# Kernel tuning notes

Measured on AMD Instinct MI355X. Metric: run time of the kernel, lower is better.

The kernel has to match this reference:

```python
import jax, jax.numpy as jnp
import numpy as np

BS, LS, HS, P, M, V, D = 16, 128, 768, 8, 1024, 20000, 512
T = BS * LS
N_POS_TOTAL = 12   # pos ids >= P are non-target (copied through)
N_PRIVACY = 4      # pos ids < N_PRIVACY count as privacy terms
TEMP = 1.0


def setup_inputs() -> dict:
    key = jax.random.key(0)
    ks = jax.random.split(key, 8)
    return {
        "inp_word": jax.random.randint(ks[0], (BS, LS), 0, V),
        "inp_pos": jax.random.randint(ks[1], (BS, LS), 0, N_POS_TOTAL),
        "inp_mask": jnp.ones((BS, LS), dtype=bool),
        "ctx": jax.random.normal(ks[2], (BS, LS, HS), dtype=jnp.float32),
        "dec_W": jax.random.normal(ks[3], (P, HS, M), dtype=jnp.float32) * 0.05,
        "dec_b": jnp.zeros((P, M), dtype=jnp.float32),
        "psr_weight": jax.random.normal(ks[4], (V, D), dtype=jnp.float32) * 0.1,
        "atk_weight": jax.random.normal(ks[5], (V, D), dtype=jnp.float32) * 0.1,
        "words": jax.random.randint(ks[6], (P, M), 0, V),
        "u_gumbel": jax.random.uniform(ks[7], (T, M), dtype=jnp.float32),
    }


def reference(inp_word, inp_pos, inp_mask, ctx, dec_W, dec_b,
              psr_weight, atk_weight, words, u_gumbel):
    bs, ls = inp_word.shape
    t_tok = bs * ls
    wordf = inp_word.reshape(t_tok)          # [T]
    posf = inp_pos.reshape(t_tok)            # [T]
    ctxf = ctx.reshape(t_tok, -1)            # [T, hs]

    # per-expert decode: Linear + LogSoftmax over each expert's sub-vocab
    logits = jnp.einsum('th,phm->ptm', ctxf, dec_W) + dec_b[:, None, :]  # [P,T,M]
    pspt = jax.nn.log_softmax(logits, axis=-1)                            # [P,T,M]

    # entropy: for each POS, mean of -pspt*exp(pspt) over its masked tokens
    neg_ent = -(pspt * jnp.exp(pspt)).sum(-1)                 # [P,T]
    pm = posf[None, :] == jnp.arange(P)[:, None]              # [P,T] token->expert mask
    n_p = pm.sum(1)                                           # [P]
    ent_p = (neg_ent * pm).sum(1) / (jnp.maximum(n_p, 1) * M)
    entropy = jnp.where(n_p > 0, ent_p, 0.0).sum()

    # gumbel-softmax sample (soft), one noise draw per token
    u = jnp.clip(u_gumbel, 1e-6, 1.0 - 1e-6)
    g = -jnp.log(-jnp.log(u))                                 # [T,M]
    spt = jax.nn.softmax((pspt + g[None]) / TEMP, axis=-1)    # [P,T,M]

    # hard word choice + soft embedding mix
    idx = jnp.argmax(spt, axis=-1)                            # [P,T]
    spt_word = jnp.take_along_axis(words, idx, axis=1)        # [P,T]
    psr_lut = psr_weight[words]                               # [P,M,D]
    atk_lut = atk_weight[words]                               # [P,M,D]
    psr_e = jnp.einsum('ptm,pmd->ptd', spt, psr_lut)          # [P,T,D]
    atk_e = jnp.einsum('ptm,pmd->ptd', spt, atk_lut)          # [P,T,D]

    # combine: each token takes its own POS expert's output (scatter)
    tmask = posf < P                                          # [T] obfuscated tokens
    sel = jnp.where(tmask, posf, 0)                           # [T] expert id
    ar = jnp.arange(t_tok)
    obf_wordf = jnp.where(tmask, spt_word[sel, ar], wordf)
    obf_psr = jnp.where(tmask[:, None], psr_e[sel, ar], psr_weight[wordf])
    obf_atk = jnp.where(tmask[:, None], atk_e[sel, ar], atk_weight[wordf])

    obf_word = obf_wordf.reshape(bs, ls)
    obf_psr_emb = obf_psr.reshape(bs, ls, -1)
    obf_atk_emb = obf_atk.reshape(bs, ls, -1)
    cpy_mask = (obf_word == inp_word) & inp_mask
    obf_mask = tmask.reshape(bs, ls)
    pri_mask = (inp_pos < N_PRIVACY) & obf_mask
    ent_loss = -entropy
    return obf_word, obf_psr_emb, obf_atk_emb, ent_loss, cpy_mask, obf_mask, pri_mask
```

## Files before the change

### kernel.cpp

```cpp
#include <hip/hip_runtime.h>
#include <cstdint>

#define BSZ   16
#define LSEQ  128
#define HS    768
#define NEXP  8
#define MM    1024
#define DD    512
#define TT    (BSZ*LSEQ)
#define NPRIV 4

#define OFF_WORD 0
#define OFF_PSR  2048
#define OFF_ATK  (2048 + 2048*512)
#define OFF_ENT  (OFF_ATK + 2048*512)
#define OFF_CPY  (OFF_ENT + 1)
#define OFF_OBF  (OFF_CPY + 2048)
#define OFF_PRI  (OFF_OBF + 2048)

#define WS_SPT      0
#define WS_TOKLIST  (TT*MM*4)
#define WS_CNT      (WS_TOKLIST + NEXP*TT*4)
#define WS_ENTSUM   (WS_CNT + NEXP*4)

__global__ void k_bucket(const int* __restrict__ pos,
                         int* __restrict__ toklist, int* __restrict__ cnt)
{
  int t = blockIdx.x * blockDim.x + threadIdx.x;
  if (t >= TT) return;
  int p = pos[t];
  if (p < NEXP) {
    int r = atomicAdd(&cnt[p], 1);
    toklist[p * TT + r] = t;
  }
}

#define TM1 32
#define TN1 128
#define TK1 64

__global__ __launch_bounds__(256) void k_decode(
    const float* __restrict__ ctx, const float* __restrict__ dec_W,
    const float* __restrict__ dec_b, const int* __restrict__ toklist,
    const int* __restrict__ cnt, float* __restrict__ logits)
{
  const int p = blockIdx.z;
  const int ncnt = cnt[p];
  const int row0 = blockIdx.y * TM1;
  if (row0 >= ncnt) return;
  const int n0 = blockIdx.x * TN1;
  const int tid = threadIdx.x;

  __shared__ float sA[TM1][TK1 + 1];
  __shared__ float sB[TK1][TN1];

  const int tx = tid & 31, ty = tid >> 5;
  const int tx4 = tx * 4, ty4 = ty * 4;

  const int ar = tid >> 3;
  const int ac0 = (tid & 7) * 8;
  int tA = -1;
  if (row0 + ar < ncnt) tA = toklist[p * TT + row0 + ar];

  const int br = tid >> 5;
  const int bc4 = (tid & 31) * 4;

  int tO[4];
  #pragma unroll
  for (int i = 0; i < 4; ++i) {
    int rr = row0 + ty4 + i;
    tO[i] = (rr < ncnt) ? toklist[p * TT + rr] : -1;
  }

  float acc[4][4] = {};

  for (int k0 = 0; k0 < HS; k0 += TK1) {
    if (tA >= 0) {
      const float* src = ctx + (size_t)tA * HS + k0 + ac0;
      #pragma unroll
      for (int j = 0; j < 8; ++j) sA[ar][ac0 + j] = src[j];
    } else {
      #pragma unroll
      for (int j = 0; j < 8; ++j) sA[ar][ac0 + j] = 0.f;
    }
    const float* wbase = dec_W + ((size_t)p * HS + k0) * MM + n0;
    #pragma unroll
    for (int j = 0; j < 8; ++j) {
      *(float4*)&sB[br + j * 8][bc4] =
          *(const float4*)(wbase + (size_t)(br + j * 8) * MM + bc4);
    }
    __syncthreads();
    #pragma unroll 8
    for (int kk = 0; kk < TK1; ++kk) {
      const float a0 = sA[ty4 + 0][kk];
      const float a1 = sA[ty4 + 1][kk];
      const float a2 = sA[ty4 + 2][kk];
      const float a3 = sA[ty4 + 3][kk];
      const float4 b = *(const float4*)&sB[kk][tx4];
      acc[0][0] = fmaf(a0, b.x, acc[0][0]); acc[0][1] = fmaf(a0, b.y, acc[0][1]);
      acc[0][2] = fmaf(a0, b.z, acc[0][2]); acc[0][3] = fmaf(a0, b.w, acc[0][3]);
      acc[1][0] = fmaf(a1, b.x, acc[1][0]); acc[1][1] = fmaf(a1, b.y, acc[1][1]);
      acc[1][2] = fmaf(a1, b.z, acc[1][2]); acc[1][3] = fmaf(a1, b.w, acc[1][3]);
      acc[2][0] = fmaf(a2, b.x, acc[2][0]); acc[2][1] = fmaf(a2, b.y, acc[2][1]);
      acc[2][2] = fmaf(a2, b.z, acc[2][2]); acc[2][3] = fmaf(a2, b.w, acc[2][3]);
      acc[3][0] = fmaf(a3, b.x, acc[3][0]); acc[3][1] = fmaf(a3, b.y, acc[3][1]);
      acc[3][2] = fmaf(a3, b.z, acc[3][2]); acc[3][3] = fmaf(a3, b.w, acc[3][3]);
    }
    __syncthreads();
  }

  const float4 bv = *(const float4*)(dec_b + (size_t)p * MM + n0 + tx4);
  #pragma unroll
  for (int i = 0; i < 4; ++i) {
    if (tO[i] >= 0) {
      float4 o;
      o.x = acc[i][0] + bv.x; o.y = acc[i][1] + bv.y;
      o.z = acc[i][2] + bv.z; o.w = acc[i][3] + bv.w;
      *(float4*)(logits + (size_t)tO[i] * MM + n0 + tx4) = o;
    }
  }
}

__device__ __forceinline__ float wred_max(float v) {
  #pragma unroll
  for (int o = 32; o > 0; o >>= 1) v = fmaxf(v, __shfl_xor(v, o));
  return v;
}
__device__ __forceinline__ float wred_sum(float v) {
  #pragma unroll
  for (int o = 32; o > 0; o >>= 1) v += __shfl_xor(v, o);
  return v;
}

__global__ __launch_bounds__(256) void k_softmax(
    const int* __restrict__ inp_word, const int* __restrict__ inp_pos,
    const int* __restrict__ inp_mask, const float* __restrict__ u_gum,
    const int* __restrict__ words,
    const float* __restrict__ psr_w, const float* __restrict__ atk_w,
    float* __restrict__ spt, float* __restrict__ entsum,
    float* __restrict__ out)
{
  const int t = blockIdx.x;
  const int tid = threadIdx.x;
  const int p = inp_pos[t];
  const int w_in = inp_word[t];
  const int msk = inp_mask[t];

  if (p >= NEXP) {
    if (tid < DD / 4) {
      const float4* pr = (const float4*)(psr_w + (size_t)w_in * DD);
      const float4* aw = (const float4*)(atk_w + (size_t)w_in * DD);
      ((float4*)(out + OFF_PSR + (size_t)t * DD))[tid] = pr[tid];
      ((float4*)(out + OFF_ATK + (size_t)t * DD))[tid] = aw[tid];
    }
    if (tid == 0) {
      out[OFF_WORD + t] = (float)w_in;
      out[OFF_CPY + t] = (msk != 0) ? 1.f : 0.f;
      out[OFF_OBF + t] = 0.f;
      out[OFF_PRI + t] = 0.f;
    }
    return;
  }

  float* lg = spt + (size_t)t * MM;
  const float4 l4 = *(const float4*)(lg + tid * 4);
  float l[4] = {l4.x, l4.y, l4.z, l4.w};

  __shared__ float sred[4];
  __shared__ float svv[4];
  __shared__ int   svi[4];

  float v = fmaxf(fmaxf(l[0], l[1]), fmaxf(l[2], l[3]));
  v = wred_max(v);
  if ((tid & 63) == 0) sred[tid >> 6] = v;
  __syncthreads();
  const float lmax = fmaxf(fmaxf(sred[0], sred[1]), fmaxf(sred[2], sred[3]));

  float e[4], ls = 0.f;
  #pragma unroll
  for (int j = 0; j < 4; ++j) { e[j] = expf(l[j] - lmax); ls += e[j]; }
  ls = wred_sum(ls);
  __syncthreads();
  if ((tid & 63) == 0) sred[tid >> 6] = ls;
  __syncthreads();
  const float s1 = sred[0] + sred[1] + sred[2] + sred[3];
  const float lse = logf(s1);

  float pe = 0.f;
  #pragma unroll
  for (int j = 0; j < 4; ++j) pe += (l[j] - lmax - lse) * e[j];
  pe = wred_sum(pe);
  __syncthreads();
  if ((tid & 63) == 0) sred[tid >> 6] = pe;
  __syncthreads();
  if (tid == 0) {
    const float tot = (sred[0] + sred[1] + sred[2] + sred[3]) / s1;
    atomicAdd(&entsum[p], -tot);
  }

  const float4 u4 = *(const float4*)(u_gum + (size_t)t * MM + tid * 4);
  float uu[4] = {u4.x, u4.y, u4.z, u4.w};
  float z[4];
  #pragma unroll
  for (int j = 0; j < 4; ++j) {
    float u = fminf(fmaxf(uu[j], 1e-6f), 1.0f - 1e-6f);
    z[j] = l[j] - logf(-logf(u));
  }

  float zv = z[0]; int zi = tid * 4;
  #pragma unroll
  for (int j = 1; j < 4; ++j) { if (z[j] > zv) { zv = z[j]; zi = tid * 4 + j; } }
  #pragma unroll
  for (int o = 32; o > 0; o >>= 1) {
    float ov = __shfl_xor(zv, o);
    int   oi = __shfl_xor(zi, o);
    if (ov > zv || (ov == zv && oi < zi)) { zv = ov; zi = oi; }
  }
  if ((tid & 63) == 0) { svv[tid >> 6] = zv; svi[tid >> 6] = zi; }
  __syncthreads();
  float fv = svv[0]; int fi = svi[0];
  #pragma unroll
  for (int q = 1; q < 4; ++q) {
    if (svv[q] > fv || (svv[q] == fv && svi[q] < fi)) { fv = svv[q]; fi = svi[q]; }
  }

  float e2[4], ls2 = 0.f;
  #pragma unroll
  for (int j = 0; j < 4; ++j) { e2[j] = expf(z[j] - fv); ls2 += e2[j]; }
  ls2 = wred_sum(ls2);
  __syncthreads();
  if ((tid & 63) == 0) sred[tid >> 6] = ls2;
  __syncthreads();
  const float s2 = sred[0] + sred[1] + sred[2] + sred[3];

  float4 o4;
  o4.x = e2[0] / s2; o4.y = e2[1] / s2; o4.z = e2[2] / s2; o4.w = e2[3] / s2;
  *(float4*)(lg + tid * 4) = o4;

  if (tid == 0) {
    const int wsel = words[p * MM + fi];
    out[OFF_WORD + t] = (float)wsel;
    out[OFF_CPY + t] = ((wsel == w_in) && (msk != 0)) ? 1.f : 0.f;
    out[OFF_OBF + t] = 1.f;
    out[OFF_PRI + t] = (p < NPRIV) ? 1.f : 0.f;
  }
}

#define TM3 32
#define TN3 64
#define TK3 64

__global__ __launch_bounds__(256) void k_embed(
    const float* __restrict__ spt, const int* __restrict__ words,
    const float* __restrict__ psr_w, const float* __restrict__ atk_w,
    const int* __restrict__ toklist, const int* __restrict__ cnt,
    float* __restrict__ out)
{
  const int p = blockIdx.z;
  const int ncnt = cnt[p];
  const int row0 = blockIdx.y * TM3;
  if (row0 >= ncnt) return;
  const int n0 = blockIdx.x * TN3;
  const int tid = threadIdx.x;

  __shared__ float sS[TM3][TK3 + 1];
  __shared__ float sP[TK3][68];
  __shared__ float sAk[TK3][68];

  const int tx = tid & 15, ty = tid >> 4;
  const int tx4 = tx * 4, ty2 = ty * 2;

  const int ar = tid >> 3;
  const int ac0 = (tid & 7) * 8;
  int tS = -1;
  if (row0 + ar < ncnt) tS = toklist[p * TT + row0 + ar];

  const int lr = tid >> 4;
  const int lc4 = (tid & 15) * 4;

  int tO[2];
  #pragma unroll
  for (int i = 0; i < 2; ++i) {
    int rr = row0 + ty2 + i;
    tO[i] = (rr < ncnt) ? toklist[p * TT + rr] : -1;
  }

  float ap[2][4] = {};
  float aa[2][4] = {};

  for (int m0 = 0; m0 < MM; m0 += TK3) {
    if (tS >= 0) {
      const float* src = spt + (size_t)tS * MM + m0 + ac0;
      #pragma unroll
      for (int j = 0; j < 8; ++j) sS[ar][ac0 + j] = src[j];
    } else {
      #pragma unroll
      for (int j = 0; j < 8; ++j) sS[ar][ac0 + j] = 0.f;
    }
    #pragma unroll
    for (int j = 0; j < 4; ++j) {
      const int r = lr + j * 16;
      const int w = words[p * MM + m0 + r];
      *(float4*)&sP[r][lc4]  = *(const float4*)(psr_w + (size_t)w * DD + n0 + lc4);
      *(float4*)&sAk[r][lc4] = *(const float4*)(atk_w + (size_t)w * DD + n0 + lc4);
    }
    __syncthreads();
    #pragma unroll 8
    for (int kk = 0; kk < TK3; ++kk) {
      const float s0 = sS[ty2 + 0][kk];
      const float s1 = sS[ty2 + 1][kk];
      const float4 pv = *(const float4*)&sP[kk][tx4];
      const float4 av = *(const float4*)&sAk[kk][tx4];
      ap[0][0] = fmaf(s0, pv.x, ap[0][0]); ap[0][1] = fmaf(s0, pv.y, ap[0][1]);
      ap[0][2] = fmaf(s0, pv.z, ap[0][2]); ap[0][3] = fmaf(s0, pv.w, ap[0][3]);
      ap[1][0] = fmaf(s1, pv.x, ap[1][0]); ap[1][1] = fmaf(s1, pv.y, ap[1][1]);
      ap[1][2] = fmaf(s1, pv.z, ap[1][2]); ap[1][3] = fmaf(s1, pv.w, ap[1][3]);
      aa[0][0] = fmaf(s0, av.x, aa[0][0]); aa[0][1] = fmaf(s0, av.y, aa[0][1]);
      aa[0][2] = fmaf(s0, av.z, aa[0][2]); aa[0][3] = fmaf(s0, av.w, aa[0][3]);
      aa[1][0] = fmaf(s1, av.x, aa[1][0]); aa[1][1] = fmaf(s1, av.y, aa[1][1]);
      aa[1][2] = fmaf(s1, av.z, aa[1][2]); aa[1][3] = fmaf(s1, av.w, aa[1][3]);
    }
    __syncthreads();
  }

  #pragma unroll
  for (int i = 0; i < 2; ++i) {
    if (tO[i] >= 0) {
      *(float4*)(out + OFF_PSR + (size_t)tO[i] * DD + n0 + tx4) =
          make_float4(ap[i][0], ap[i][1], ap[i][2], ap[i][3]);
      *(float4*)(out + OFF_ATK + (size_t)tO[i] * DD + n0 + tx4) =
          make_float4(aa[i][0], aa[i][1], aa[i][2], aa[i][3]);
    }
  }
}

__global__ void k_finalize(const float* __restrict__ entsum,
                           const int* __restrict__ cnt, float* __restrict__ out)
{
  if (threadIdx.x == 0 && blockIdx.x == 0) {
    float s = 0.f;
    for (int p = 0; p < NEXP; ++p) {
      int n = cnt[p];
      if (n > 0) s += entsum[p] / ((float)n * (float)MM);
    }
    out[OFF_ENT] = -s;
  }
}

extern "C" void kernel_launch(void* const* d_in, const int* in_sizes, int n_in,
                              void* d_out, int out_size, void* d_ws, size_t ws_size,
                              hipStream_t stream)
{
  (void)in_sizes; (void)n_in; (void)out_size; (void)ws_size;

  const int*   inp_word = (const int*)d_in[0];
  const int*   inp_pos  = (const int*)d_in[1];
  const int*   inp_mask = (const int*)d_in[2];
  const float* ctx      = (const float*)d_in[3];
  const float* dec_W    = (const float*)d_in[4];
  const float* dec_b    = (const float*)d_in[5];
  const float* psr_w    = (const float*)d_in[6];
  const float* atk_w    = (const float*)d_in[7];
  const int*   words    = (const int*)d_in[8];
  const float* u_gum    = (const float*)d_in[9];

  float* out = (float*)d_out;
  char*  ws  = (char*)d_ws;
  float* spt     = (float*)(ws + WS_SPT);
  int*   toklist = (int*)(ws + WS_TOKLIST);
  int*   cnt     = (int*)(ws + WS_CNT);
  float* entsum  = (float*)(ws + WS_ENTSUM);

  hipMemsetAsync(ws + WS_CNT, 0, NEXP * 4 * 2, stream);
  k_bucket<<<TT / 256, 256, 0, stream>>>(inp_pos, toklist, cnt);
  k_decode<<<dim3(MM / TN1, TT / TM1, NEXP), 256, 0, stream>>>(
      ctx, dec_W, dec_b, toklist, cnt, spt);
  k_softmax<<<TT, 256, 0, stream>>>(
      inp_word, inp_pos, inp_mask, u_gum, words, psr_w, atk_w, spt, entsum, out);
  k_embed<<<dim3(DD / TN3, TT / TM3, NEXP), 256, 0, stream>>>(
      spt, words, psr_w, atk_w, toklist, cnt, out);
  k_finalize<<<1, 64, 0, stream>>>(entsum, cnt, out);
}
```

Measured before the change: 338.3 us.

## Register-prefetch next tiles in decode and embed GEMMs; split embed by table

Both the decode GEMM and the embedding GEMM now load the next K-tile from global memory into registers while the current shared-memory tile is being computed, hiding global load latency with single-stage software pipelining. The embed kernel is also split so each block handles only one lookup table (psr or atk), doubling the grid and halving shared memory and accumulators per block. This should raise occupancy and overlap, at the cost of reading the spt tile twice and holding more registers for the prefetch buffers.

Measured after the change: 407.7 us. +20.5%, slower.

```diff
diff --git a/kernel.cpp b/kernel.cpp
--- a/kernel.cpp
+++ b/kernel.cpp
@@ -72,24 +72,40 @@
     tO[i] = (rr < ncnt) ? toklist[p * TT + rr] : -1;
   }
 
-  float acc[4][4] = {};
-
-  for (int k0 = 0; k0 < HS; k0 += TK1) {
+  float  aReg[8];
+  float4 bReg[8];
+
+  auto loadA = [&](int k0) {
     if (tA >= 0) {
       const float* src = ctx + (size_t)tA * HS + k0 + ac0;
       #pragma unroll
-      for (int j = 0; j < 8; ++j) sA[ar][ac0 + j] = src[j];
+      for (int j = 0; j < 8; ++j) aReg[j] = src[j];
     } else {
       #pragma unroll
-      for (int j = 0; j < 8; ++j) sA[ar][ac0 + j] = 0.f;
-    }
+      for (int j = 0; j < 8; ++j) aReg[j] = 0.f;
+    }
+  };
+  auto loadB = [&](int k0) {
     const float* wbase = dec_W + ((size_t)p * HS + k0) * MM + n0;
     #pragma unroll
-    for (int j = 0; j < 8; ++j) {
-      *(float4*)&sB[br + j * 8][bc4] =
-          *(const float4*)(wbase + (size_t)(br + j * 8) * MM + bc4);
-    }
+    for (int j = 0; j < 8; ++j)
+      bReg[j] = *(const float4*)(wbase + (size_t)(br + j * 8) * MM + bc4);
+  };
+
+  float acc[4][4] = {};
+
+  loadA(0);
+  loadB(0);
+
+  for (int k0 = 0; k0 < HS; k0 += TK1) {
+    #pragma unroll
+    for (int j = 0; j < 8; ++j) sA[ar][ac0 + j] = aReg[j];
+    #pragma unroll
+    for (int j = 0; j < 8; ++j) *(float4*)&sB[br + j * 8][bc4] = bReg[j];
     __syncthreads();
+
+    if (k0 + TK1 < HS) { loadA(k0 + TK1); loadB(k0 + TK1); }
+
     #pragma unroll 8
     for (int kk = 0; kk < TK1; ++kk) {
       const float a0 = sA[ty4 + 0][kk];
@@ -260,12 +276,15 @@
   const int ncnt = cnt[p];
   const int row0 = blockIdx.y * TM3;
   if (row0 >= ncnt) return;
-  const int n0 = blockIdx.x * TN3;
+  const int table = blockIdx.x & 1;
+  const int n0 = (blockIdx.x >> 1) * TN3;
   const int tid = threadIdx.x;
 
+  const float* lut = table ? atk_w : psr_w;
+  const size_t out_off = table ? OFF_ATK : OFF_PSR;
+
   __shared__ float sS[TM3][TK3 + 1];
-  __shared__ float sP[TK3][68];
-  __shared__ float sAk[TK3][68];
+  __shared__ float sL[TK3][68];
 
   const int tx = tid & 15, ty = tid >> 4;
   const int tx4 = tx * 4, ty2 = ty * 2;
@@ -285,40 +304,50 @@
     tO[i] = (rr < ncnt) ? toklist[p * TT + rr] : -1;
   }
 
-  float ap[2][4] = {};
-  float aa[2][4] = {};
-
-  for (int m0 = 0; m0 < MM; m0 += TK3) {
+  float  sReg[8];
+  float4 lReg[4];
+
+  auto loadS = [&](int m0) {
     if (tS >= 0) {
       const float* src = spt + (size_t)tS * MM + m0 + ac0;
       #pragma unroll
-      for (int j = 0; j < 8; ++j) sS[ar][ac0 + j] = src[j];
+      for (int j = 0; j < 8; ++j) sReg[j] = src[j];
     } else {
       #pragma unroll
-      for (int j = 0; j < 8; ++j) sS[ar][ac0 + j] = 0.f;
-    }
+      for (int j = 0; j < 8; ++j) sReg[j] = 0.f;
+    }
+  };
+  auto loadL = [&](int m0) {
     #pragma unroll
     for (int j = 0; j < 4; ++j) {
-      const int r = lr + j * 16;
-      const int w = words[p * MM + m0 + r];
-      *(float4*)&sP[r][lc4]  = *(const float4*)(psr_w + (size_t)w * DD + n0 + lc4);
-      *(float4*)&sAk[r][lc4] = *(const float4*)(atk_w + (size_t)w * DD + n0 + lc4);
-    }
+      const int w = words[p * MM + m0 + lr + j * 16];
+      lReg[j] = *(const float4*)(lut + (size_t)w * DD + n0 + lc4);
+    }
+  };
+
+  float acc[2][4] = {};
+
+  loadS(0);
+  loadL(0);
+
+  for (int m0 = 0; m0 < MM; m0 += TK3) {
+    #pragma unroll
+    for (int j = 0; j < 8; ++j) sS[ar][ac0 + j] = sReg[j];
+    #pragma unroll
+    for (int j = 0; j < 4; ++j) *(float4*)&sL[lr + j * 16][lc4] = lReg[j];
     __syncthreads();
+
+    if (m0 + TK3 < MM) { loadS(m0 + TK3); loadL(m0 + TK3); }
+
     #pragma unroll 8
     for (int kk = 0; kk < TK3; ++kk) {
       const float s0 = sS[ty2 + 0][kk];
       const float s1 = sS[ty2 + 1][kk];
-      const float4 pv = *(const float4*)&sP[kk][tx4];
-      const float4 av = *(const float4*)&sAk[kk][tx4];
-      ap[0][0] = fmaf(s0, pv.x, ap[0][0]); ap[0][1] = fmaf(s0, pv.y, ap[0][1]);
-      ap[0][2] = fmaf(s0, pv.z, ap[0][2]); ap[0][3] = fmaf(s0, pv.w, ap[0][3]);
-      ap[1][0] = fmaf(s1, pv.x, ap[1][0]); ap[1][1] = fmaf(s1, pv.y, ap[1][1]);
-      ap[1][2] = fmaf(s1, pv.z, ap[1][2]); ap[1][3] = fmaf(s1, pv.w, ap[1][3]);
-      aa[0][0] = fmaf(s0, av.x, aa[0][0]); aa[0][1] = fmaf(s0, av.y, aa[0][1]);
-      aa[0][2] = fmaf(s0, av.z, aa[0][2]); aa[0][3] = fmaf(s0, av.w, aa[0][3]);
-      aa[1][0] = fmaf(s1, av.x, aa[1][0]); aa[1][1] = fmaf(s1, av.y, aa[1][1]);
-      aa[1][2] = fmaf(s1, av.z, aa[1][2]); aa[1][3] = fmaf(s1, av.w, aa[1][3]);
+      const float4 lv = *(const float4*)&sL[kk][tx4];
+      acc[0][0] = fmaf(s0, lv.x, acc[0][0]); acc[0][1] = fmaf(s0, lv.y, acc[0][1]);
+      acc[0][2] = fmaf(s0, lv.z, acc[0][2]); acc[0][3] = fmaf(s0, lv.w, acc[0][3]);
+      acc[1][0] = fmaf(s1, lv.x, acc[1][0]); acc[1][1] = fmaf(s1, lv.y, acc[1][1]);
+      acc[1][2] = fmaf(s1, lv.z, acc[1][2]); acc[1][3] = fmaf(s1, lv.w, acc[1][3]);
     }
     __syncthreads();
   }
@@ -326,10 +355,8 @@
   #pragma unroll
   for (int i = 0; i < 2; ++i) {
     if (tO[i] >= 0) {
-      *(float4*)(out + OFF_PSR + (size_t)tO[i] * DD + n0 + tx4) =
-          make_float4(ap[i][0], ap[i][1], ap[i][2], ap[i][3]);
-      *(float4*)(out + OFF_ATK + (size_t)tO[i] * DD + n0 + tx4) =
-          make_float4(aa[i][0], aa[i][1], aa[i][2], aa[i][3]);
+      *(float4*)(out + out_off + (size_t)tO[i] * DD + n0 + tx4) =
+          make_float4(acc[i][0], acc[i][1], acc[i][2], acc[i][3]);
     }
   }
 }
@@ -377,7 +404,7 @@
       ctx, dec_W, dec_b, toklist, cnt, spt);
   k_softmax<<<TT, 256, 0, stream>>>(
       inp_word, inp_pos, inp_mask, u_gum, words, psr_w, atk_w, spt, entsum, out);
-  k_embed<<<dim3(DD / TN3, TT / TM3, NEXP), 256, 0, stream>>>(
+  k_embed<<<dim3(2 * (DD / TN3), TT / TM3, NEXP), 256, 0, stream>>>(
       spt, words, psr_w, atk_w, toklist, cnt, out);
   k_finalize<<<1, 64, 0, stream>>>(entsum, cnt, out);
 }
```

## Split-K decode and embed GEMMs with atomic accumulation and register prefetch

Applied to the files above, without the earlier changes.

Both grouped GEMMs (decode logits and embedding mix) now split their reduction dimension four ways across extra blocks and accumulate partial results with float atomicAdd into zero-initialised buffers. The bias add moves into the softmax kernel. Global loads are double-buffered through registers with a smaller K tile. The aim is to fill the GPU with more blocks and hide load latency, at the cost of two large memsets, atomic traffic, and non-deterministic summation order.

Measured after the change: 375.5 us. +11.0%, slower.

```diff
diff --git a/kernel.cpp b/kernel.cpp
--- a/kernel.cpp
+++ b/kernel.cpp
@@ -37,33 +37,38 @@
 
 #define TM1 32
 #define TN1 128
-#define TK1 64
-
-__global__ __launch_bounds__(256) void k_decode(
+#define TK1 32
+#define NSK 4
+
+__global__ __launch_bounds__(256, 4) void k_decode(
     const float* __restrict__ ctx, const float* __restrict__ dec_W,
-    const float* __restrict__ dec_b, const int* __restrict__ toklist,
-    const int* __restrict__ cnt, float* __restrict__ logits)
-{
-  const int p = blockIdx.z;
+    const int* __restrict__ toklist, const int* __restrict__ cnt,
+    float* __restrict__ logits)
+{
+  const int p  = blockIdx.z >> 2;
+  const int ks = blockIdx.z & 3;
   const int ncnt = cnt[p];
   const int row0 = blockIdx.y * TM1;
   if (row0 >= ncnt) return;
   const int n0 = blockIdx.x * TN1;
+  const int kb = ks * (HS / NSK);
   const int tid = threadIdx.x;
 
-  __shared__ float sA[TM1][TK1 + 1];
+  __shared__ float sA[TM1][TK1 + 4];
   __shared__ float sB[TK1][TN1];
 
   const int tx = tid & 31, ty = tid >> 5;
   const int tx4 = tx * 4, ty4 = ty * 4;
 
   const int ar = tid >> 3;
-  const int ac0 = (tid & 7) * 8;
+  const int ac = (tid & 7) * 4;
   int tA = -1;
   if (row0 + ar < ncnt) tA = toklist[p * TT + row0 + ar];
+  const float* aSrc = (tA >= 0) ? (ctx + (size_t)tA * HS + kb + ac) : nullptr;
 
   const int br = tid >> 5;
   const int bc4 = (tid & 31) * 4;
+  const float* bSrc = dec_W + ((size_t)p * HS + kb) * MM + n0 + bc4;
 
   int tO[4];
   #pragma unroll
@@ -72,24 +77,32 @@
     tO[i] = (rr < ncnt) ? toklist[p * TT + rr] : -1;
   }
 
+  float4 aP = (tA >= 0) ? *(const float4*)aSrc : make_float4(0.f, 0.f, 0.f, 0.f);
+  float4 bP0 = *(const float4*)(bSrc + (size_t)(br +  0) * MM);
+  float4 bP1 = *(const float4*)(bSrc + (size_t)(br +  8) * MM);
+  float4 bP2 = *(const float4*)(bSrc + (size_t)(br + 16) * MM);
+  float4 bP3 = *(const float4*)(bSrc + (size_t)(br + 24) * MM);
+
   float acc[4][4] = {};
 
-  for (int k0 = 0; k0 < HS; k0 += TK1) {
-    if (tA >= 0) {
-      const float* src = ctx + (size_t)tA * HS + k0 + ac0;
-      #pragma unroll
-      for (int j = 0; j < 8; ++j) sA[ar][ac0 + j] = src[j];
-    } else {
-      #pragma unroll
-      for (int j = 0; j < 8; ++j) sA[ar][ac0 + j] = 0.f;
-    }
-    const float* wbase = dec_W + ((size_t)p * HS + k0) * MM + n0;
-    #pragma unroll
-    for (int j = 0; j < 8; ++j) {
-      *(float4*)&sB[br + j * 8][bc4] =
-          *(const float4*)(wbase + (size_t)(br + j * 8) * MM + bc4);
-    }
+  for (int k0 = 0; k0 < HS / NSK; k0 += TK1) {
+    *(float4*)&sA[ar][ac] = aP;
+    *(float4*)&sB[br +  0][bc4] = bP0;
+    *(float4*)&sB[br +  8][bc4] = bP1;
+    *(float4*)&sB[br + 16][bc4] = bP2;
+    *(float4*)&sB[br + 24][bc4] = bP3;
     __syncthreads();
+
+    if (k0 + TK1 < HS / NSK) {
+      const int kn = k0 + TK1;
+      if (tA >= 0) aP = *(const float4*)(aSrc + kn);
+      const float* bn = bSrc + (size_t)kn * MM;
+      bP0 = *(const float4*)(bn + (size_t)(br +  0) * MM);
+      bP1 = *(const float4*)(bn + (size_t)(br +  8) * MM);
+      bP2 = *(const float4*)(bn + (size_t)(br + 16) * MM);
+      bP3 = *(const float4*)(bn + (size_t)(br + 24) * MM);
+    }
+
     #pragma unroll 8
     for (int kk = 0; kk < TK1; ++kk) {
       const float a0 = sA[ty4 + 0][kk];
@@ -109,14 +122,14 @@
     __syncthreads();
   }
 
-  const float4 bv = *(const float4*)(dec_b + (size_t)p * MM + n0 + tx4);
   #pragma unroll
   for (int i = 0; i < 4; ++i) {
     if (tO[i] >= 0) {
-      float4 o;
-      o.x = acc[i][0] + bv.x; o.y = acc[i][1] + bv.y;
-      o.z = acc[i][2] + bv.z; o.w = acc[i][3] + bv.w;
-      *(float4*)(logits + (size_t)tO[i] * MM + n0 + tx4) = o;
+      float* dst = logits + (size_t)tO[i] * MM + n0 + tx4;
+      atomicAdd(dst + 0, acc[i][0]);
+      atomicAdd(dst + 1, acc[i][1]);
+      atomicAdd(dst + 2, acc[i][2]);
+      atomicAdd(dst + 3, acc[i][3]);
     }
   }
 }
@@ -135,7 +148,7 @@
 __global__ __launch_bounds__(256) void k_softmax(
     const int* __restrict__ inp_word, const int* __restrict__ inp_pos,
     const int* __restrict__ inp_mask, const float* __restrict__ u_gum,
-    const int* __restrict__ words,
+    const int* __restrict__ words, const float* __restrict__ dec_b,
     const float* __restrict__ psr_w, const float* __restrict__ atk_w,
     float* __restrict__ spt, float* __restrict__ entsum,
     float* __restrict__ out)
@@ -164,7 +177,8 @@
 
   float* lg = spt + (size_t)t * MM;
   const float4 l4 = *(const float4*)(lg + tid * 4);
-  float l[4] = {l4.x, l4.y, l4.z, l4.w};
+  const float4 b4 = *(const float4*)(dec_b + (size_t)p * MM + tid * 4);
+  float l[4] = {l4.x + b4.x, l4.y + b4.y, l4.z + b4.z, l4.w + b4.w};
 
   __shared__ float sred[4];
   __shared__ float svv[4];
@@ -248,35 +262,39 @@
 
 #define TM3 32
 #define TN3 64
-#define TK3 64
-
-__global__ __launch_bounds__(256) void k_embed(
+#define TK3 32
+#define NSM 4
+
+__global__ __launch_bounds__(256, 4) void k_embed(
     const float* __restrict__ spt, const int* __restrict__ words,
     const float* __restrict__ psr_w, const float* __restrict__ atk_w,
     const int* __restrict__ toklist, const int* __restrict__ cnt,
     float* __restrict__ out)
 {
-  const int p = blockIdx.z;
+  const int p  = blockIdx.z >> 2;
+  const int ms = blockIdx.z & 3;
   const int ncnt = cnt[p];
   const int row0 = blockIdx.y * TM3;
   if (row0 >= ncnt) return;
   const int n0 = blockIdx.x * TN3;
+  const int mb = ms * (MM / NSM);
   const int tid = threadIdx.x;
 
-  __shared__ float sS[TM3][TK3 + 1];
-  __shared__ float sP[TK3][68];
-  __shared__ float sAk[TK3][68];
+  __shared__ float sS[TM3][TK3 + 4];
+  __shared__ float sL[2][TK3][68];
 
   const int tx = tid & 15, ty = tid >> 4;
   const int tx4 = tx * 4, ty2 = ty * 2;
 
   const int ar = tid >> 3;
-  const int ac0 = (tid & 7) * 8;
+  const int ac = (tid & 7) * 4;
   int tS = -1;
   if (row0 + ar < ncnt) tS = toklist[p * TT + row0 + ar];
+  const float* sSrc = (tS >= 0) ? (spt + (size_t)tS * MM + mb + ac) : nullptr;
 
   const int lr = tid >> 4;
   const int lc4 = (tid & 15) * 4;
+  const int* wRow = words + p * MM + mb + lr;
 
   int tO[2];
   #pragma unroll
@@ -285,32 +303,40 @@
     tO[i] = (rr < ncnt) ? toklist[p * TT + rr] : -1;
   }
 
+  float4 sP = (tS >= 0) ? *(const float4*)sSrc : make_float4(0.f, 0.f, 0.f, 0.f);
+  int w0 = wRow[0], w1 = wRow[16];
+  float4 lp0 = *(const float4*)(psr_w + (size_t)w0 * DD + n0 + lc4);
+  float4 lp1 = *(const float4*)(psr_w + (size_t)w1 * DD + n0 + lc4);
+  float4 la0 = *(const float4*)(atk_w + (size_t)w0 * DD + n0 + lc4);
+  float4 la1 = *(const float4*)(atk_w + (size_t)w1 * DD + n0 + lc4);
+
   float ap[2][4] = {};
   float aa[2][4] = {};
 
-  for (int m0 = 0; m0 < MM; m0 += TK3) {
-    if (tS >= 0) {
-      const float* src = spt + (size_t)tS * MM + m0 + ac0;
-      #pragma unroll
-      for (int j = 0; j < 8; ++j) sS[ar][ac0 + j] = src[j];
-    } else {
-      #pragma unroll
-      for (int j = 0; j < 8; ++j) sS[ar][ac0 + j] = 0.f;
-    }
-    #pragma unroll
-    for (int j = 0; j < 4; ++j) {
-      const int r = lr + j * 16;
-      const int w = words[p * MM + m0 + r];
-      *(float4*)&sP[r][lc4]  = *(const float4*)(psr_w + (size_t)w * DD + n0 + lc4);
-      *(float4*)&sAk[r][lc4] = *(const float4*)(atk_w + (size_t)w * DD + n0 + lc4);
-    }
+  for (int m0 = 0; m0 < MM / NSM; m0 += TK3) {
+    *(float4*)&sS[ar][ac] = sP;
+    *(float4*)&sL[0][lr +  0][lc4] = lp0;
+    *(float4*)&sL[0][lr + 16][lc4] = lp1;
+    *(float4*)&sL[1][lr +  0][lc4] = la0;
+    *(float4*)&sL[1][lr + 16][lc4] = la1;
     __syncthreads();
+
+    if (m0 + TK3 < MM / NSM) {
+      const int mn = m0 + TK3;
+      if (tS >= 0) sP = *(const float4*)(sSrc + mn);
+      w0 = wRow[mn]; w1 = wRow[mn + 16];
+      lp0 = *(const float4*)(psr_w + (size_t)w0 * DD + n0 + lc4);
+      lp1 = *(const float4*)(psr_w + (size_t)w1 * DD + n0 + lc4);
+      la0 = *(const float4*)(atk_w + (size_t)w0 * DD + n0 + lc4);
+      la1 = *(const float4*)(atk_w + (size_t)w1 * DD + n0 + lc4);
+    }
+
     #pragma unroll 8
     for (int kk = 0; kk < TK3; ++kk) {
       const float s0 = sS[ty2 + 0][kk];
       const float s1 = sS[ty2 + 1][kk];
-      const float4 pv = *(const float4*)&sP[kk][tx4];
-      const float4 av = *(const float4*)&sAk[kk][tx4];
+      const float4 pv = *(const float4*)&sL[0][kk][tx4];
+      const float4 av = *(const float4*)&sL[1][kk][tx4];
       ap[0][0] = fmaf(s0, pv.x, ap[0][0]); ap[0][1] = fmaf(s0, pv.y, ap[0][1]);
       ap[0][2] = fmaf(s0, pv.z, ap[0][2]); ap[0][3] = fmaf(s0, pv.w, ap[0][3]);
       ap[1][0] = fmaf(s1, pv.x, ap[1][0]); ap[1][1] = fmaf(s1, pv.y, ap[1][1]);
@@ -326,10 +352,12 @@
   #pragma unroll
   for (int i = 0; i < 2; ++i) {
     if (tO[i] >= 0) {
-      *(float4*)(out + OFF_PSR + (size_t)tO[i] * DD + n0 + tx4) =
-          make_float4(ap[i][0], ap[i][1], ap[i][2], ap[i][3]);
-      *(float4*)(out + OFF_ATK + (size_t)tO[i] * DD + n0 + tx4) =
-          make_float4(aa[i][0], aa[i][1], aa[i][2], aa[i][3]);
+      float* dp = out + OFF_PSR + (size_t)tO[i] * DD + n0 + tx4;
+      float* da = out + OFF_ATK + (size_t)tO[i] * DD + n0 + tx4;
+      atomicAdd(dp + 0, ap[i][0]); atomicAdd(dp + 1, ap[i][1]);
+      atomicAdd(dp + 2, ap[i][2]); atomicAdd(dp + 3, ap[i][3]);
+      atomicAdd(da + 0, aa[i][0]); atomicAdd(da + 1, aa[i][1]);
+      atomicAdd(da + 2, aa[i][2]); atomicAdd(da + 3, aa[i][3]);
     }
   }
 }
@@ -372,12 +400,15 @@
   float* entsum  = (float*)(ws + WS_ENTSUM);
 
   hipMemsetAsync(ws + WS_CNT, 0, NEXP * 4 * 2, stream);
+  hipMemsetAsync(spt, 0, (size_t)TT * MM * 4, stream);
+  hipMemsetAsync(out + OFF_PSR, 0, (size_t)2 * 2048 * 512 * 4, stream);
+
   k_bucket<<<TT / 256, 256, 0, stream>>>(inp_pos, toklist, cnt);
-  k_decode<<<dim3(MM / TN1, TT / TM1, NEXP), 256, 0, stream>>>(
-      ctx, dec_W, dec_b, toklist, cnt, spt);
+  k_decode<<<dim3(MM / TN1, TT / TM1, NEXP * NSK), 256, 0, stream>>>(
+      ctx, dec_W, toklist, cnt, spt);
   k_softmax<<<TT, 256, 0, stream>>>(
-      inp_word, inp_pos, inp_mask, u_gum, words, psr_w, atk_w, spt, entsum, out);
-  k_embed<<<dim3(DD / TN3, TT / TM3, NEXP), 256, 0, stream>>>(
+      inp_word, inp_pos, inp_mask, u_gum, words, dec_b, psr_w, atk_w, spt, entsum, out);
+  k_embed<<<dim3(DD / TN3, TT / TM3, NEXP * NSM), 256, 0, stream>>>(
       spt, words, psr_w, atk_w, toklist, cnt, out);
   k_finalize<<<1, 64, 0, stream>>>(entsum, cnt, out);
 }
```
